# Kernel tuning notes

Measured on AMD Instinct MI355X. Metric: run time of the kernel, lower is better.

Reference implementation:

```python
import jax, jax.numpy as jnp
import numpy as np
from jax import lax

E, H, I, K, T = 16, 2048, 1408, 2, 8192


def setup_inputs() -> dict:
    key = jax.random.key(0)
    k1, k2, k3, k4, k5 = jax.random.split(key, 5)
    hidden_states = jax.random.normal(k1, (T, H), dtype=jnp.float32)
    top_k_index = jax.random.randint(k2, (T, K), 0, E, dtype=jnp.int64)
    top_k_weights = jax.random.uniform(k3, (T, K), dtype=jnp.float32)
    gate_up_proj = jax.random.normal(k4, (E, 2 * I, H), dtype=jnp.float32) * 0.02
    down_proj = jax.random.normal(k5, (E, H, I), dtype=jnp.float32) * 0.02
    return {
        "hidden_states": hidden_states,
        "top_k_index": top_k_index,
        "top_k_weights": top_k_weights,
        "gate_up_proj": gate_up_proj,
        "down_proj": down_proj,
    }


def _moe_forward(hidden_states, top_k_index, top_k_weights, gate_up_proj, down_proj):
    # Combine weight per (expert, token): sum over top-k slots where the slot
    # routes to that expert. Tokens not routed to an expert get weight 0, so the
    # dense per-expert GEMM below computes the exact same math as the gather/
    # scatter-add loop in the original module (masking is linear post-GEMM).
    one_hot = jax.nn.one_hot(top_k_index, E, dtype=top_k_weights.dtype)  # [T,K,E]
    combine = jnp.einsum("tke,tk->et", one_hot, top_k_weights)           # [E,T]

    def expert_step(acc, xs):
        w_gu, w_d, cw = xs                      # [2I,H], [H,I], [T]
        gu = hidden_states @ w_gu.T             # [T,2I]
        gate, up = jnp.split(gu, 2, axis=-1)    # chunk(2, dim=-1)
        h = jax.nn.silu(gate) * up              # SwiGLU
        out = h @ w_d.T                         # [T,H]
        return acc + out * cw[:, None], None

    acc0 = jnp.zeros_like(hidden_states)
    final, _ = lax.scan(expert_step, acc0, (gate_up_proj, down_proj, combine))
    return final


def reference(hidden_states, top_k_index, top_k_weights, gate_up_proj, down_proj):
    return _moe_forward(hidden_states, top_k_index, top_k_weights, gate_up_proj, down_proj)
```

## Files before the change

kernel.cpp:

```cpp
#include <hip/hip_runtime.h>

#define E_ 16
#define H_ 2048
#define I_ 1408
#define TWOI_ 2816
#define K_ 2
#define T_ 8192
#define TK_ 16384

typedef unsigned short ushort_t;
typedef unsigned int uint_t;
typedef short short8 __attribute__((ext_vector_type(8)));
typedef float f32x4 __attribute__((ext_vector_type(4)));

#define AS1 __attribute__((address_space(1)))
#define AS3 __attribute__((address_space(3)))

__device__ __forceinline__ void gl2lds16(const ushort_t* g, ushort_t* l) {
    __builtin_amdgcn_global_load_lds((const AS1 uint_t*)g, (AS3 uint_t*)l, 16, 0, 0);
}

__device__ __forceinline__ ushort_t f2bf(float f) {
    uint_t u = __float_as_uint(f);
    u += 0x7fffu + ((u >> 16) & 1u);
    return (ushort_t)(u >> 16);
}
__device__ __forceinline__ uint_t pack2(float a, float b) {
    return (uint_t)f2bf(a) | ((uint_t)f2bf(b) << 16);
}
__device__ __forceinline__ float bflo(uint_t v) { return __uint_as_float(v << 16); }
__device__ __forceinline__ float bfhi(uint_t v) { return __uint_as_float(v & 0xffff0000u); }

__global__ void routing_kernel(const int* __restrict__ idx32,
                               const float* __restrict__ wts,
                               int* __restrict__ meta,
                               int* __restrict__ token_ids,
                               int* __restrict__ row_of_slot) {
    __shared__ int s_cnt[E_], s_off[E_ + 1], s_cur[E_], s_orodd;
    const int tid = threadIdx.x;
    if (tid < E_) { s_cnt[tid] = 0; s_cur[tid] = 0; }
    if (tid == 0) s_orodd = 0;
    __syncthreads();
    int ao = 0;
    for (int s = tid; s < TK_ / 2; s += (int)blockDim.x) ao |= idx32[2 * s + 1];
    atomicOr(&s_orodd, ao);
    __syncthreads();
    const bool is64 = (s_orodd == 0);
    for (int s = tid; s < TK_; s += (int)blockDim.x) {
        int e = is64 ? idx32[2 * s] : idx32[s];
        atomicAdd(&s_cnt[e], 1);
    }
    __syncthreads();
    if (tid == 0) {
        int acc = 0, nt = 0;
        for (int e = 0; e < E_; e++) {
            s_off[e] = acc;
            meta[1 + e] = acc;
            for (int m = 0; m < s_cnt[e]; m += 256) {
                meta[32 + nt] = e;
                meta[192 + nt] = acc + m;
                nt++;
            }
            acc += s_cnt[e];
        }
        s_off[E_] = acc;
        meta[1 + E_] = acc;
        meta[0] = nt;
    }
    __syncthreads();
    for (int s = tid; s < TK_; s += (int)blockDim.x) {
        int e = is64 ? idx32[2 * s] : idx32[s];
        int p = atomicAdd(&s_cur[e], 1);
        int r = s_off[e] + p;
        token_ids[r] = s >> 1;
        row_of_slot[s] = r;
    }
}

__global__ void f2bf_kernel(const float* __restrict__ src, ushort_t* __restrict__ dst, int n8) {
    int i = blockIdx.x * blockDim.x + threadIdx.x;
    const int stride = gridDim.x * blockDim.x;
    for (; i < n8; i += stride) {
        const float4* s = (const float4*)src + 2 * (size_t)i;
        float4 a = s[0], b = s[1];
        uint4 o;
        o.x = pack2(a.x, a.y);
        o.y = pack2(a.z, a.w);
        o.z = pack2(b.x, b.y);
        o.w = pack2(b.z, b.w);
        ((uint4*)dst)[i] = o;
    }
}

__global__ void f2bf_gu_kernel(const float* __restrict__ src, ushort_t* __restrict__ dst) {
    const int PER_E = TWOI_ * (H_ / 8);
    const int n8 = E_ * PER_E;
    int i = blockIdx.x * blockDim.x + threadIdx.x;
    const int stride = gridDim.x * blockDim.x;
    for (; i < n8; i += stride) {
        int e = i / PER_E;
        int rem = i % PER_E;
        int r = rem / (H_ / 8);
        int cg = rem % (H_ / 8);
        int pr;
        if (r < I_) pr = 32 * (r >> 4) + (r & 15);
        else { int r2 = r - I_; pr = 32 * (r2 >> 4) + 16 + (r2 & 15); }
        const float4* s = (const float4*)src + 2 * (size_t)i;
        float4 a = s[0], b = s[1];
        uint4 o;
        o.x = pack2(a.x, a.y);
        o.y = pack2(a.z, a.w);
        o.z = pack2(b.x, b.y);
        o.w = pack2(b.z, b.w);
        *(uint4*)(dst + ((size_t)e * TWOI_ + pr) * H_ + cg * 8) = o;
    }
}

template <int NCOLS, int KDIM, int MODE>
__global__ __launch_bounds__(512, 2) void moe_gemm(
    const ushort_t* __restrict__ A, const ushort_t* __restrict__ Bw,
    const int* __restrict__ meta, const int* __restrict__ token_ids,
    ushort_t* __restrict__ Obf) {
    extern __shared__ ushort_t sh[];
    constexpr int NT = KDIM / 64;
    static_assert(NT % 2 == 0, "K-tile count must be even");
    constexpr int TILEE = 256 * 64;
    constexpr int BUFE = 2 * TILEE;

    const int ny = NCOLS / 256;
    const int nx = meta[0];
    const int nwg = nx * ny;
    int flat = blockIdx.x;
    if (flat >= nwg) return;
    {
        const int q = nwg >> 3, r = nwg & 7;
        const int x = flat & 7, i = flat >> 3;
        flat = (x < r ? x * (q + 1) : r * (q + 1) + (x - r) * q) + i;
    }
    const int GRP = 4;
    const int gid = flat / (GRP * ny), rem = flat % (GRP * ny);
    const int gx = min(GRP, nx - gid * GRP);
    const int bx = gid * GRP + rem % gx;
    const int by = rem / gx;

    const int e = meta[32 + bx];
    const int row0 = meta[192 + bx];
    const int rend = meta[2 + e];
    const int mrows = min(256, rend - row0);
    const int n0 = by * 256;
    const int tid = threadIdx.x;
    const int lane = tid & 63, wid = tid >> 6;
    const int wr = wid >> 2, wc = wid & 3;

    const int l8 = lane >> 3;
    const int srcswz = ((lane & 7) ^ l8) << 3;
    const int ldst = wid * 512;
    const ushort_t* Be = Bw + (size_t)e * NCOLS * KDIM;
    const ushort_t* apt[4];
    const ushort_t* bpt[4];
#pragma unroll
    for (int c = 0; c < 4; c++) {
        const int ra = c * 64 + wid * 8 + l8;
        const int rc = min(ra, mrows - 1);
        const long arow = (MODE == 0) ? (long)token_ids[row0 + rc] : (long)(row0 + rc);
        apt[c] = A + arow * KDIM + srcswz;
        bpt[c] = Be + (size_t)(n0 + ra) * KDIM + srcswz;
    }

    auto stage = [&](int bsel) {
        ushort_t* ab = sh + bsel * BUFE;
#pragma unroll
        for (int c = 0; c < 4; c++) {
            gl2lds16(apt[c], ab + c * 4096 + ldst);
            gl2lds16(bpt[c], ab + TILEE + c * 4096 + ldst);
            apt[c] += 64; bpt[c] += 64;
        }
    };

    f32x4 acc[8][4];
#pragma unroll
    for (int i = 0; i < 8; i++)
#pragma unroll
        for (int j = 0; j < 4; j++) acc[i][j] = (f32x4){0.f, 0.f, 0.f, 0.f};

    const int fr = lane & 15;
    const int axm = (fr & 7) << 3;
    const int k0 = ((lane >> 4) * 8) ^ axm;
    const int k1 = (((lane >> 4) * 8) + 32) ^ axm;

    stage(0);
    stage(1);
    asm volatile("s_waitcnt vmcnt(8)" ::: "memory");
    __builtin_amdgcn_sched_barrier(0);
    __builtin_amdgcn_s_barrier();
    __builtin_amdgcn_sched_barrier(0);

    auto body = [&](int bsel, int t) {
        const ushort_t* af_base = sh + bsel * BUFE + (wr * 128 + fr) * 64;
        const ushort_t* bf_base = sh + bsel * BUFE + TILEE + (wc * 64 + fr) * 64;
        short8 bfr[4][2], af[4][2];
#pragma unroll
        for (int nt = 0; nt < 4; nt++) {
            bfr[nt][0] = *(const short8*)(bf_base + nt * 1024 + k0);
            bfr[nt][1] = *(const short8*)(bf_base + nt * 1024 + k1);
        }
#pragma unroll
        for (int mt = 0; mt < 4; mt++) {
            af[mt][0] = *(const short8*)(af_base + mt * 1024 + k0);
            af[mt][1] = *(const short8*)(af_base + mt * 1024 + k1);
        }
        __builtin_amdgcn_s_setprio(1);
#pragma unroll
        for (int mt = 0; mt < 4; mt++)
#pragma unroll
            for (int nt = 0; nt < 4; nt++) {
                acc[mt][nt] = __builtin_amdgcn_mfma_f32_16x16x32_bf16(af[mt][0], bfr[nt][0], acc[mt][nt], 0, 0, 0);
                acc[mt][nt] = __builtin_amdgcn_mfma_f32_16x16x32_bf16(af[mt][1], bfr[nt][1], acc[mt][nt], 0, 0, 0);
            }
        __builtin_amdgcn_s_setprio(0);
#pragma unroll
        for (int mt = 0; mt < 4; mt++) {
            af[mt][0] = *(const short8*)(af_base + 4096 + mt * 1024 + k0);
            af[mt][1] = *(const short8*)(af_base + 4096 + mt * 1024 + k1);
        }
        __builtin_amdgcn_sched_barrier(0);
        asm volatile("s_waitcnt lgkmcnt(0)" ::: "memory");
        __builtin_amdgcn_sched_barrier(0);
        __builtin_amdgcn_s_barrier();
        __builtin_amdgcn_sched_barrier(0);
        if (t + 2 < NT) stage(bsel);
        __builtin_amdgcn_s_setprio(1);
#pragma unroll
        for (int mt = 0; mt < 4; mt++)
#pragma unroll
            for (int nt = 0; nt < 4; nt++) {
                acc[4 + mt][nt] = __builtin_amdgcn_mfma_f32_16x16x32_bf16(af[mt][0], bfr[nt][0], acc[4 + mt][nt], 0, 0, 0);
                acc[4 + mt][nt] = __builtin_amdgcn_mfma_f32_16x16x32_bf16(af[mt][1], bfr[nt][1], acc[4 + mt][nt], 0, 0, 0);
            }
        __builtin_amdgcn_s_setprio(0);
        __builtin_amdgcn_sched_barrier(0);
        if (t + 2 < NT)
            asm volatile("s_waitcnt vmcnt(8)" ::: "memory");
        else
            asm volatile("s_waitcnt vmcnt(0)" ::: "memory");
        __builtin_amdgcn_sched_barrier(0);
        __builtin_amdgcn_s_barrier();
        __builtin_amdgcn_sched_barrier(0);
    };

#pragma unroll 1
    for (int tt = 0; tt < NT; tt += 2) {
        body(0, tt);
        body(1, tt + 1);
    }

    const int quad = lane >> 4, tn = lane & 15;
    if (MODE == 0) {
        const int hbase = ((n0 + wc * 64) >> 1) + tn;
#pragma unroll
        for (int mt = 0; mt < 8; mt++) {
#pragma unroll
            for (int reg = 0; reg < 4; reg++) {
                const int rl = wr * 128 + mt * 16 + quad * 4 + reg;
                if (rl < mrows) {
                    ushort_t* dst = Obf + (size_t)(row0 + rl) * I_ + hbase;
#pragma unroll
                    for (int j = 0; j < 2; j++) {
                        float g = acc[mt][2 * j][reg];
                        float u = acc[mt][2 * j + 1][reg];
                        float h = g / (1.f + __expf(-g)) * u;
                        dst[j * 16] = f2bf(h);
                    }
                }
            }
        }
    } else {
#pragma unroll
        for (int mt = 0; mt < 8; mt++) {
#pragma unroll
            for (int reg = 0; reg < 4; reg++) {
                const int rl = wr * 128 + mt * 16 + quad * 4 + reg;
                if (rl < mrows) {
                    ushort_t* dst = Obf + (size_t)(row0 + rl) * NCOLS + n0 + wc * 64 + tn;
#pragma unroll
                    for (int nt = 0; nt < 4; nt++) dst[nt * 16] = f2bf(acc[mt][nt][reg]);
                }
            }
        }
    }
}

__global__ void combine_kernel(const ushort_t* __restrict__ Y,
                               const int* __restrict__ row_of_slot,
                               const float* __restrict__ wts,
                               float* __restrict__ out) {
    const int n8 = T_ * (H_ / 8);
    int i = blockIdx.x * blockDim.x + threadIdx.x;
    const int stride = gridDim.x * blockDim.x;
    for (; i < n8; i += stride) {
        const int t = i / (H_ / 8);
        const int c = (i % (H_ / 8)) * 8;
        const int r0 = row_of_slot[2 * t], r1 = row_of_slot[2 * t + 1];
        const float w0 = wts[2 * t], w1 = wts[2 * t + 1];
        const uint4 y0 = *(const uint4*)(Y + (size_t)r0 * H_ + c);
        const uint4 y1 = *(const uint4*)(Y + (size_t)r1 * H_ + c);
        const uint_t a[4] = {y0.x, y0.y, y0.z, y0.w};
        const uint_t b[4] = {y1.x, y1.y, y1.z, y1.w};
        float o[8];
#pragma unroll
        for (int j = 0; j < 4; j++) {
            o[2 * j]     = w0 * bflo(a[j]) + w1 * bflo(b[j]);
            o[2 * j + 1] = w0 * bfhi(a[j]) + w1 * bfhi(b[j]);
        }
        float4* dst = (float4*)(out + (size_t)t * H_ + c);
        dst[0] = make_float4(o[0], o[1], o[2], o[3]);
        dst[1] = make_float4(o[4], o[5], o[6], o[7]);
    }
}

extern "C" void kernel_launch(void* const* d_in, const int* in_sizes, int n_in,
                              void* d_out, int out_size, void* d_ws, size_t ws_size,
                              hipStream_t stream) {
    const float* hidden = (const float*)d_in[0];
    const int* topk_idx = (const int*)d_in[1];
    const float* topk_w = (const float*)d_in[2];
    const float* w_gu = (const float*)d_in[3];
    const float* w_d = (const float*)d_in[4];
    float* out = (float*)d_out;

    char* ws = (char*)d_ws;
    int* meta = (int*)ws;
    int* token_ids = (int*)(ws + 4096);
    int* row_of_slot = (int*)(ws + 4096 + 65536);
    ushort_t* Xb = (ushort_t*)(ws + 135168);
    ushort_t* Wgu = Xb + (size_t)T_ * H_;
    ushort_t* Wd = Wgu + (size_t)E_ * TWOI_ * H_;
    ushort_t* Hb = Wd + (size_t)E_ * H_ * I_;
    ushort_t* Y = Hb + (size_t)TK_ * I_;

    (void)hipFuncSetAttribute(reinterpret_cast<const void*>(moe_gemm<TWOI_, H_, 0>),
                              hipFuncAttributeMaxDynamicSharedMemorySize, 131072);
    (void)hipFuncSetAttribute(reinterpret_cast<const void*>(moe_gemm<H_, I_, 1>),
                              hipFuncAttributeMaxDynamicSharedMemorySize, 131072);

    routing_kernel<<<1, 1024, 0, stream>>>(topk_idx, topk_w, meta, token_ids, row_of_slot);

    f2bf_kernel<<<4096, 256, 0, stream>>>(hidden, Xb, (int)((size_t)T_ * H_ / 8));
    f2bf_gu_kernel<<<8192, 256, 0, stream>>>(w_gu, Wgu);
    f2bf_kernel<<<8192, 256, 0, stream>>>(w_d, Wd, (int)((size_t)E_ * H_ * I_ / 8));

    moe_gemm<TWOI_, H_, 0><<<80 * 11, 512, 131072, stream>>>(
        Xb, Wgu, meta, token_ids, Hb);

    moe_gemm<H_, I_, 1><<<80 * 8, 512, 131072, stream>>>(
        Hb, Wd, meta, token_ids, Y);

    combine_kernel<<<4096, 256, 0, stream>>>(Y, row_of_slot, topk_w, out);
}
```

Measured before the change: 1.081 ms.

## Switch MoE GEMM to 4-stage K=32 pipeline with one barrier per tile

Restructures the main loop from a double-buffered K=64 tile scheme with two barriers per tile into a four-slot ring of K=32 tiles, keeping three loads in flight. Each iteration issues one barrier, prefetches three tiles ahead, then reads fragments and runs the MFMAs. The LDS swizzle is changed to match the 32-wide rows. The aim is deeper global-load latency hiding and less synchronization per MFMA. The cost is more loop iterations, fewer MFMAs per barrier, and a possible hazard if the vmcnt gating is misordered.

```diff
diff --git a/kernel.cpp b/kernel.cpp
--- a/kernel.cpp
+++ b/kernel.cpp
@@ -122,10 +122,8 @@
     const int* __restrict__ meta, const int* __restrict__ token_ids,
     ushort_t* __restrict__ Obf) {
     extern __shared__ ushort_t sh[];
-    constexpr int NT = KDIM / 64;
-    static_assert(NT % 2 == 0, "K-tile count must be even");
-    constexpr int TILEE = 256 * 64;
-    constexpr int BUFE = 2 * TILEE;
+    constexpr int NT = KDIM / 32;
+    constexpr int SLOT = 16384;
 
     const int ny = NCOLS / 256;
     const int nx = meta[0];
@@ -152,29 +150,27 @@
     const int lane = tid & 63, wid = tid >> 6;
     const int wr = wid >> 2, wc = wid & 3;
 
-    const int l8 = lane >> 3;
-    const int srcswz = ((lane & 7) ^ l8) << 3;
-    const int ldst = wid * 512;
+    const int srg = wid * 16 + (lane >> 2);
+    const int scol = (((lane & 3) ^ ((lane >> 3) & 3)) * 8);
     const ushort_t* Be = Bw + (size_t)e * NCOLS * KDIM;
-    const ushort_t* apt[4];
-    const ushort_t* bpt[4];
-#pragma unroll
-    for (int c = 0; c < 4; c++) {
-        const int ra = c * 64 + wid * 8 + l8;
+    const ushort_t* ap[2];
+    const ushort_t* bp[2];
+#pragma unroll
+    for (int c = 0; c < 2; c++) {
+        const int ra = c * 128 + srg;
         const int rc = min(ra, mrows - 1);
         const long arow = (MODE == 0) ? (long)token_ids[row0 + rc] : (long)(row0 + rc);
-        apt[c] = A + arow * KDIM + srcswz;
-        bpt[c] = Be + (size_t)(n0 + ra) * KDIM + srcswz;
-    }
-
-    auto stage = [&](int bsel) {
-        ushort_t* ab = sh + bsel * BUFE;
-#pragma unroll
-        for (int c = 0; c < 4; c++) {
-            gl2lds16(apt[c], ab + c * 4096 + ldst);
-            gl2lds16(bpt[c], ab + TILEE + c * 4096 + ldst);
-            apt[c] += 64; bpt[c] += 64;
-        }
+        ap[c] = A + arow * KDIM + scol;
+        bp[c] = Be + (size_t)(n0 + ra) * KDIM + scol;
+    }
+
+    auto stage = [&](int slot) {
+        ushort_t* d = sh + slot * SLOT + wid * 512;
+        gl2lds16(ap[0], d);
+        gl2lds16(ap[1], d + 4096);
+        gl2lds16(bp[0], d + 8192);
+        gl2lds16(bp[1], d + 12288);
+        ap[0] += 32; ap[1] += 32; bp[0] += 32; bp[1] += 32;
     };
 
     f32x4 acc[8][4];
@@ -184,75 +180,59 @@
         for (int j = 0; j < 4; j++) acc[i][j] = (f32x4){0.f, 0.f, 0.f, 0.f};
 
     const int fr = lane & 15;
-    const int axm = (fr & 7) << 3;
-    const int k0 = ((lane >> 4) * 8) ^ axm;
-    const int k1 = (((lane >> 4) * 8) + 32) ^ axm;
+    const int q8 = (((lane >> 4) ^ ((fr >> 1) & 3)) * 8);
+    const int aofs = (wr * 128 + fr) * 32 + q8;
+    const int bofs = 8192 + (wc * 64 + fr) * 32 + q8;
 
     stage(0);
     stage(1);
+    stage(2);
     asm volatile("s_waitcnt vmcnt(8)" ::: "memory");
     __builtin_amdgcn_sched_barrier(0);
-    __builtin_amdgcn_s_barrier();
-    __builtin_amdgcn_sched_barrier(0);
-
-    auto body = [&](int bsel, int t) {
-        const ushort_t* af_base = sh + bsel * BUFE + (wr * 128 + fr) * 64;
-        const ushort_t* bf_base = sh + bsel * BUFE + TILEE + (wc * 64 + fr) * 64;
-        short8 bfr[4][2], af[4][2];
-#pragma unroll
-        for (int nt = 0; nt < 4; nt++) {
-            bfr[nt][0] = *(const short8*)(bf_base + nt * 1024 + k0);
-            bfr[nt][1] = *(const short8*)(bf_base + nt * 1024 + k1);
-        }
-#pragma unroll
-        for (int mt = 0; mt < 4; mt++) {
-            af[mt][0] = *(const short8*)(af_base + mt * 1024 + k0);
-            af[mt][1] = *(const short8*)(af_base + mt * 1024 + k1);
-        }
+
+    auto body = [&](int t, bool do_stage, int gate) {
+        asm volatile("s_waitcnt lgkmcnt(0)" ::: "memory");
+        __builtin_amdgcn_sched_barrier(0);
+        __builtin_amdgcn_s_barrier();
+        __builtin_amdgcn_sched_barrier(0);
+        if (do_stage) stage((t + 3) & 3);
+        __builtin_amdgcn_sched_barrier(0);
+        const ushort_t* sb = sh + (t & 3) * SLOT;
+        short8 b[4], a0[4], a1[4];
+#pragma unroll
+        for (int nt = 0; nt < 4; nt++) b[nt] = *(const short8*)(sb + bofs + nt * 512);
+#pragma unroll
+        for (int mt = 0; mt < 4; mt++) a0[mt] = *(const short8*)(sb + aofs + mt * 512);
+#pragma unroll
+        for (int mt = 0; mt < 4; mt++) a1[mt] = *(const short8*)(sb + aofs + 2048 + mt * 512);
+        __builtin_amdgcn_sched_barrier(0);
+        if (gate == 8)      asm volatile("s_waitcnt vmcnt(8)" ::: "memory");
+        else if (gate == 4) asm volatile("s_waitcnt vmcnt(4)" ::: "memory");
+        else                asm volatile("s_waitcnt vmcnt(0)" ::: "memory");
+        __builtin_amdgcn_sched_barrier(0);
         __builtin_amdgcn_s_setprio(1);
 #pragma unroll
         for (int mt = 0; mt < 4; mt++)
 #pragma unroll
-            for (int nt = 0; nt < 4; nt++) {
-                acc[mt][nt] = __builtin_amdgcn_mfma_f32_16x16x32_bf16(af[mt][0], bfr[nt][0], acc[mt][nt], 0, 0, 0);
-                acc[mt][nt] = __builtin_amdgcn_mfma_f32_16x16x32_bf16(af[mt][1], bfr[nt][1], acc[mt][nt], 0, 0, 0);
-            }
+            for (int nt = 0; nt < 4; nt++)
+                acc[mt][nt] = __builtin_amdgcn_mfma_f32_16x16x32_bf16(a0[mt], b[nt], acc[mt][nt], 0, 0, 0);
         __builtin_amdgcn_s_setprio(0);
-#pragma unroll
-        for (int mt = 0; mt < 4; mt++) {
-            af[mt][0] = *(const short8*)(af_base + 4096 + mt * 1024 + k0);
-            af[mt][1] = *(const short8*)(af_base + 4096 + mt * 1024 + k1);
-        }
-        __builtin_amdgcn_sched_barrier(0);
-        asm volatile("s_waitcnt lgkmcnt(0)" ::: "memory");
-        __builtin_amdgcn_sched_barrier(0);
-        __builtin_amdgcn_s_barrier();
-        __builtin_amdgcn_sched_barrier(0);
-        if (t + 2 < NT) stage(bsel);
+        __builtin_amdgcn_sched_barrier(0);
         __builtin_amdgcn_s_setprio(1);
 #pragma unroll
         for (int mt = 0; mt < 4; mt++)
 #pragma unroll
-            for (int nt = 0; nt < 4; nt++) {
-                acc[4 + mt][nt] = __builtin_amdgcn_mfma_f32_16x16x32_bf16(af[mt][0], bfr[nt][0], acc[4 + mt][nt], 0, 0, 0);
-                acc[4 + mt][nt] = __builtin_amdgcn_mfma_f32_16x16x32_bf16(af[mt][1], bfr[nt][1], acc[4 + mt][nt], 0, 0, 0);
-            }
+            for (int nt = 0; nt < 4; nt++)
+                acc[4 + mt][nt] = __builtin_amdgcn_mfma_f32_16x16x32_bf16(a1[mt], b[nt], acc[4 + mt][nt], 0, 0, 0);
         __builtin_amdgcn_s_setprio(0);
         __builtin_amdgcn_sched_barrier(0);
-        if (t + 2 < NT)
-            asm volatile("s_waitcnt vmcnt(8)" ::: "memory");
-        else
-            asm volatile("s_waitcnt vmcnt(0)" ::: "memory");
-        __builtin_amdgcn_sched_barrier(0);
-        __builtin_amdgcn_s_barrier();
-        __builtin_amdgcn_sched_barrier(0);
     };
 
 #pragma unroll 1
-    for (int tt = 0; tt < NT; tt += 2) {
-        body(0, tt);
-        body(1, tt + 1);
-    }
+    for (int t = 0; t < NT - 3; ++t) body(t, true, 8);
+    body(NT - 3, false, 4);
+    body(NT - 2, false, 0);
+    body(NT - 1, false, 0);
 
     const int quad = lane >> 4, tn = lane & 15;
     if (MODE == 0) {
```

New measurement: 1.085 ms. No clear change (+0.3%).
